# Performance work log

Hardware: AMD Instinct MI355X
Metric: run time of the kernel (lower is better)

Reference implementation:

```python
import jax, jax.numpy as jnp
import numpy as np

VOCAB, EMB, HID, LAYERS = 32000, 512, 512, 2
B, S = 16, 256


def setup_inputs() -> dict:
    key = jax.random.key(0)
    ks = jax.random.split(key, 8)
    x = jax.random.randint(ks[0], (B, S), 0, VOCAB)
    emb = jax.random.normal(ks[1], (VOCAB, EMB), dtype=jnp.float32) * 0.02
    # input_dim == hidden_dim == 512, so per-layer weights can be stacked
    Wih = jax.random.normal(ks[2], (LAYERS, 4 * HID, EMB), dtype=jnp.float32) * 0.05
    Whh = jax.random.normal(ks[3], (LAYERS, 4 * HID, HID), dtype=jnp.float32) * 0.05
    b = jax.random.normal(ks[4], (LAYERS, 4 * HID), dtype=jnp.float32) * 0.05
    fc_w = jax.random.normal(ks[5], (VOCAB, HID), dtype=jnp.float32) * 0.02
    fc_b = jnp.zeros((VOCAB,), dtype=jnp.float32)
    return {"x": x, "emb": emb, "Wih": Wih, "Whh": Whh, "b": b, "fc_w": fc_w, "fc_b": fc_b}


def reference(x, emb, Wih, Whh, b, fc_w, fc_b):
    L = Wih.shape[0]
    Bsz = x.shape[0]
    H = Whh.shape[-1]
    xe = emb[x]  # (B, S, E)
    h0 = jnp.zeros((L, Bsz, H), dtype=emb.dtype)
    c0 = jnp.zeros((L, Bsz, H), dtype=emb.dtype)

    def step(carry, xt):  # xt: (B, E)
        h, c = carry
        inp = xt
        hs, cs = [], []
        for l in range(L):  # small fixed layer loop
            gates = inp @ Wih[l].T + h[l] @ Whh[l].T + b[l]  # (B, 4H)
            i, f, g, o = jnp.split(gates, 4, axis=1)
            cn = jax.nn.sigmoid(f) * c[l] + jax.nn.sigmoid(i) * jnp.tanh(g)
            hn = jax.nn.sigmoid(o) * jnp.tanh(cn)
            hs.append(hn)
            cs.append(cn)
            inp = hn
        return (jnp.stack(hs), jnp.stack(cs)), inp

    _, outs = jax.lax.scan(step, (h0, c0), jnp.swapaxes(xe, 0, 1))  # outs: (S, B, H)
    outs = jnp.swapaxes(outs, 0, 1)  # (B, S, H); dropout is identity (eval)
    logits = outs @ fc_w.T + fc_b  # (B, S, V)
    return logits
```

## Files before the change

kernel.cpp:

```cpp
#include <hip/hip_runtime.h>
#include <hip/hip_bf16.h>

#define SEQ 256
#define NB 16
#define HID 512
#define VOC 32000

typedef short bf16x8 __attribute__((ext_vector_type(8)));
typedef float f32x4 __attribute__((ext_vector_type(4)));
typedef unsigned long long u64;

__device__ __forceinline__ void ld_lds16(const void* g, void* l) {
  __builtin_amdgcn_global_load_lds((const __attribute__((address_space(1))) void*)g,
                                   (__attribute__((address_space(3))) void*)l, 16, 0, 0);
}

__device__ __forceinline__ float sigf(float x) { return 1.0f / (1.0f + expf(-x)); }

__device__ __forceinline__ unsigned pk2(float a, float b) {
  __hip_bfloat16 ha = __float2bfloat16(a), hb = __float2bfloat16(b);
  unsigned short ua = *(unsigned short*)&ha, ub = *(unsigned short*)&hb;
  return (unsigned)ua | ((unsigned)ub << 16);
}

__device__ __forceinline__ u64 agload(const u64* p) {
  return __hip_atomic_load(p, __ATOMIC_RELAXED, __HIP_MEMORY_SCOPE_AGENT);
}
__device__ __forceinline__ void agstore(u64* p, u64 v) {
  __hip_atomic_store(p, v, __ATOMIC_RELAXED, __HIP_MEMORY_SCOPE_AGENT);
}

__device__ __forceinline__ void issue16(u64* q, const u64* base) {
#pragma unroll
  for (int s = 0; s < 4; ++s)
#pragma unroll
    for (int j = 0; j < 4; ++j) q[s * 4 + j] = agload(base + s * 256 + j * 16);
}
__device__ __forceinline__ void revalidate16(u64* q, const u64* base, unsigned tg) {
  for (;;) {
    int bad = 0;
#pragma unroll
    for (int i = 0; i < 16; ++i) bad |= ((unsigned)(q[i] >> 32) != tg);
    if (!__any(bad)) break;
    __builtin_amdgcn_s_sleep(1);
#pragma unroll
    for (int i = 0; i < 16; ++i)
      if ((unsigned)(q[i] >> 32) != tg)
        q[i] = agload(base + (i >> 2) * 256 + (i & 3) * 16);
  }
}

__device__ __forceinline__ void cvt8_hilo(const float* p, bf16x8* h8, bf16x8* l8) {
  union { unsigned short u[8]; bf16x8 v; } uh, ul;
#pragma unroll
  for (int i = 0; i < 8; ++i) {
    float v = p[i];
    __hip_bfloat16 h = __float2bfloat16(v);
    uh.u[i] = *(unsigned short*)&h;
    float rem = v - __bfloat162float(h);
    __hip_bfloat16 l = __float2bfloat16(rem);
    ul.u[i] = *(unsigned short*)&l;
  }
  *h8 = uh.v;
  *l8 = ul.v;
}

__global__ void embed_k(const int* __restrict__ x, const float* __restrict__ emb,
                        unsigned short* __restrict__ xe) {
  int bid = blockIdx.x;
  int t = bid >> 4, b = bid & 15;
  int tok = x[b * SEQ + t];
  const float4* src = (const float4*)(emb + (size_t)tok * HID);
  int e = threadIdx.x;
  float4 a = src[e * 2], c = src[e * 2 + 1];
  uint4 o;
  o.x = pk2(a.x, a.y); o.y = pk2(a.z, a.w);
  o.z = pk2(c.x, c.y); o.w = pk2(c.z, c.w);
  ((uint4*)(xe + (size_t)bid * HID))[e] = o;
}

__global__ void cvt_k(const float* __restrict__ in, uint4* __restrict__ out) {
  size_t i = (size_t)blockIdx.x * blockDim.x + threadIdx.x;
  const float4* in4 = (const float4*)in;
  float4 a = in4[i * 2], b = in4[i * 2 + 1];
  uint4 o;
  o.x = pk2(a.x, a.y); o.y = pk2(a.z, a.w);
  o.z = pk2(b.x, b.y); o.w = pk2(b.z, b.w);
  out[i] = o;
}

__global__ __launch_bounds__(256) void gx_gemm(const __hip_bfloat16* __restrict__ A,
                                               const __hip_bfloat16* __restrict__ Bw,
                                               unsigned short* __restrict__ C) {
  __shared__ __align__(16) unsigned short lds_a[128 * 32];
  __shared__ __align__(16) unsigned short lds_b[128 * 32];
  const int tid = threadIdx.x;
  const int lane = tid & 63, wid = tid >> 6;
  const int m0 = blockIdx.y * 128, n0 = blockIdx.x * 128;
  const char* Ab = (const char*)A;
  const char* Bb = (const char*)Bw;
  const int ra = tid >> 2, cb = (tid & 3) * 16;
  f32x4 acc[4][4] = {};
  const int wm = (wid >> 1) * 64, wn = (wid & 1) * 64;
  const int fr = lane & 15, fk = (lane >> 4) * 8;
  for (int k0 = 0; k0 < HID; k0 += 32) {
    ld_lds16(Ab + (size_t)(m0 + ra) * 1024 + k0 * 2 + cb, (char*)lds_a + wid * 1024);
    ld_lds16(Ab + (size_t)(m0 + 64 + ra) * 1024 + k0 * 2 + cb, (char*)lds_a + 4096 + wid * 1024);
    ld_lds16(Bb + (size_t)(n0 + ra) * 1024 + k0 * 2 + cb, (char*)lds_b + wid * 1024);
    ld_lds16(Bb + (size_t)(n0 + 64 + ra) * 1024 + k0 * 2 + cb, (char*)lds_b + 4096 + wid * 1024);
    __syncthreads();
    bf16x8 af[4], bf[4];
#pragma unroll
    for (int i = 0; i < 4; ++i) af[i] = *(const bf16x8*)&lds_a[(wm + i * 16 + fr) * 32 + fk];
#pragma unroll
    for (int j = 0; j < 4; ++j) bf[j] = *(const bf16x8*)&lds_b[(wn + j * 16 + fr) * 32 + fk];
#pragma unroll
    for (int i = 0; i < 4; ++i)
#pragma unroll
      for (int j = 0; j < 4; ++j)
        acc[i][j] = __builtin_amdgcn_mfma_f32_16x16x32_bf16(af[i], bf[j], acc[i][j], 0, 0, 0);
    __syncthreads();
  }
  const int cr = (lane >> 4) * 4, cc = lane & 15;
#pragma unroll
  for (int i = 0; i < 4; ++i)
#pragma unroll
    for (int jj = 0; jj < 4; ++jj) {
      size_t base = (size_t)(m0 + wm + i * 16 + cr) * 2048 + (n0 + wn + jj * 16 + cc);
#pragma unroll
      for (int r = 0; r < 4; ++r) {
        __hip_bfloat16 h = __float2bfloat16(acc[i][jj][r]);
        C[base + (size_t)r * 2048] = *(unsigned short*)&h;
      }
    }
}

__global__ __launch_bounds__(256) void lstm_k(
    const float* __restrict__ Wih, const float* __restrict__ Whh,
    const float* __restrict__ bias, const unsigned short* __restrict__ gxb,
    u64* __restrict__ h0r, u64* __restrict__ h1r, unsigned short* __restrict__ outs) {
  __shared__ float pbuf[4][16][17];
  const int tid = threadIdx.x, bid = blockIdx.x;
  const int lay = bid >> 7, r8 = bid & 127;
  const int hc0 = r8 * 4;
  const int wid = tid >> 6, lane = tid & 63;
  const int b16 = lane & 15, hi = lane >> 4;

  const int jrow = (b16 >> 2) * HID + hc0 + (b16 & 3);
  const int kb = wid * 128 + hi * 8;
  const float* wih_row = Wih + ((size_t)lay * 2048 + jrow) * HID;
  const float* whh_row = Whh + ((size_t)lay * 2048 + jrow) * HID;
  bf16x8 w0[4], w1[4], w2[4], w3[4];
#pragma unroll
  for (int s = 0; s < 4; ++s) {
    if (lay == 0) {
      cvt8_hilo(whh_row + kb + s * 32, &w0[s], &w1[s]);
      w2[s] = w0[s]; w3[s] = w1[s];
    } else {
      cvt8_hilo(wih_row + kb + s * 32, &w0[s], &w1[s]);
      cvt8_hilo(whh_row + kb + s * 32, &w2[s], &w3[s]);
    }
  }
  const int eb = lane & 15, ehl = lane >> 4;
  float bq[4];
#pragma unroll
  for (int q = 0; q < 4; ++q) bq[q] = bias[lay * 2048 + q * HID + hc0 + ehl];
  float c_reg = 0.f;
  const int lbase = wid * 1024 + hi * 64 + b16;

#pragma unroll 1
  for (int t = 0; t < SEQ; ++t) {
    f32x4 acc0 = {0.f, 0.f, 0.f, 0.f}, acc1 = {0.f, 0.f, 0.f, 0.f};
    float gxr[4] = {0.f, 0.f, 0.f, 0.f};
    if (lay == 0) {
      const u64* srcA = h0r + (size_t)t * 4096 + lbase;
      u64 qa[16];
      issue16(qa, srcA);
      if (wid == 0) {
        const unsigned short* gp = gxb + ((size_t)(t * 16 + eb)) * 2048 + hc0 + ehl;
#pragma unroll
        for (int q = 0; q < 4; ++q) {
          union { unsigned u; float f; } cv;
          cv.u = (unsigned)gp[q * HID] << 16;
          gxr[q] = cv.f;
        }
        asm volatile("" : "+v"(gxr[0]), "+v"(gxr[1]), "+v"(gxr[2]), "+v"(gxr[3]));
      }
      revalidate16(qa, srcA, (unsigned)t);
#pragma unroll
      for (int s = 0; s < 4; ++s) {
        union { unsigned u[4]; bf16x8 v; } bb;
#pragma unroll
        for (int j = 0; j < 4; ++j) bb.u[j] = (unsigned)qa[s * 4 + j];
        acc0 = __builtin_amdgcn_mfma_f32_16x16x32_bf16(w0[s], bb.v, acc0, 0, 0, 0);
        acc1 = __builtin_amdgcn_mfma_f32_16x16x32_bf16(w1[s], bb.v, acc1, 0, 0, 0);
      }
    } else {
      const u64* srcA = h0r + (size_t)(t + 1) * 4096 + lbase;
      const u64* srcB = h1r + (size_t)t * 4096 + lbase;
      u64 qb[16], qa[16];
      issue16(qb, srcB);
      issue16(qa, srcA);
      revalidate16(qb, srcB, (unsigned)t);
#pragma unroll
      for (int s = 0; s < 4; ++s) {
        union { unsigned u[4]; bf16x8 v; } bb;
#pragma unroll
        for (int j = 0; j < 4; ++j) bb.u[j] = (unsigned)qb[s * 4 + j];
        acc0 = __builtin_amdgcn_mfma_f32_16x16x32_bf16(w2[s], bb.v, acc0, 0, 0, 0);
        acc1 = __builtin_amdgcn_mfma_f32_16x16x32_bf16(w3[s], bb.v, acc1, 0, 0, 0);
      }
      revalidate16(qa, srcA, (unsigned)(t + 1));
#pragma unroll
      for (int s = 0; s < 4; ++s) {
        union { unsigned u[4]; bf16x8 v; } bb;
#pragma unroll
        for (int j = 0; j < 4; ++j) bb.u[j] = (unsigned)qa[s * 4 + j];
        acc0 = __builtin_amdgcn_mfma_f32_16x16x32_bf16(w0[s], bb.v, acc0, 0, 0, 0);
        acc1 = __builtin_amdgcn_mfma_f32_16x16x32_bf16(w1[s], bb.v, acc1, 0, 0, 0);
      }
    }
    f32x4 acc = acc0 + acc1;
#pragma unroll
    for (int rr = 0; rr < 4; ++rr) pbuf[wid][hi * 4 + rr][b16] = acc[rr];
    __syncthreads();

    if (wid == 0) {
      float pre[4];
#pragma unroll
      for (int q = 0; q < 4; ++q) {
        const int rl = q * 4 + ehl;
        pre[q] = bq[q] + gxr[q] + pbuf[0][rl][eb] + pbuf[1][rl][eb] +
                 pbuf[2][rl][eb] + pbuf[3][rl][eb];
      }
      float iv = sigf(pre[0]), fv = sigf(pre[1]);
      float gv = tanhf(pre[2]), ov = sigf(pre[3]);
      c_reg = fv * c_reg + iv * gv;
      float hn = ov * tanhf(c_reg);
      __hip_bfloat16 hh = __float2bfloat16(hn);
      int hb = (int)*(unsigned short*)&hh;
      int pr = __shfl_xor(hb, 16, 64);
      unsigned data32 = (unsigned)(unsigned short)hb | ((unsigned)(unsigned short)pr << 16);
      u64* ringo = (lay ? h1r : h0r) + (size_t)(t + 1) * 4096;
      if ((ehl & 1) == 0)
        agstore(ringo + (r8 * 2 + (ehl >> 1)) * 16 + eb,
                (u64)data32 | ((u64)(unsigned)(t + 1) << 32));
      if (lay) {
        unsigned d23 = (unsigned)__shfl((int)data32, eb + 32, 64);
        if (ehl == 0)
          *(u64*)(outs + ((size_t)(t * 16 + eb)) * 512 + hc0) = (u64)data32 | ((u64)d23 << 32);
      }
    }
    __syncthreads();
  }
}

__global__ __launch_bounds__(256) void fc_gemm(const __hip_bfloat16* __restrict__ A,
                                               const __hip_bfloat16* __restrict__ Bw,
                                               const float* __restrict__ bias,
                                               float* __restrict__ C) {
  __shared__ __align__(16) unsigned short lds_a[128 * 32];
  __shared__ __align__(16) unsigned short lds_b[128 * 32];
  const int tid = threadIdx.x;
  const int lane = tid & 63, wid = tid >> 6;
  const int m0 = blockIdx.y * 128, n0 = blockIdx.x * 128;
  const char* Ab = (const char*)A;
  const char* Bb = (const char*)Bw;
  const int ra = tid >> 2, cb = (tid & 3) * 16;
  f32x4 acc[4][4] = {};
  const int wm = (wid >> 1) * 64, wn = (wid & 1) * 64;
  const int fr = lane & 15, fk = (lane >> 4) * 8;
  for (int k0 = 0; k0 < HID; k0 += 32) {
    ld_lds16(Ab + (size_t)(m0 + ra) * 1024 + k0 * 2 + cb, (char*)lds_a + wid * 1024);
    ld_lds16(Ab + (size_t)(m0 + 64 + ra) * 1024 + k0 * 2 + cb, (char*)lds_a + 4096 + wid * 1024);
    ld_lds16(Bb + (size_t)(n0 + ra) * 1024 + k0 * 2 + cb, (char*)lds_b + wid * 1024);
    ld_lds16(Bb + (size_t)(n0 + 64 + ra) * 1024 + k0 * 2 + cb, (char*)lds_b + 4096 + wid * 1024);
    __syncthreads();
    bf16x8 af[4], bf[4];
#pragma unroll
    for (int i = 0; i < 4; ++i) af[i] = *(const bf16x8*)&lds_a[(wm + i * 16 + fr) * 32 + fk];
#pragma unroll
    for (int j = 0; j < 4; ++j) bf[j] = *(const bf16x8*)&lds_b[(wn + j * 16 + fr) * 32 + fk];
#pragma unroll
    for (int i = 0; i < 4; ++i)
#pragma unroll
      for (int j = 0; j < 4; ++j)
        acc[i][j] = __builtin_amdgcn_mfma_f32_16x16x32_bf16(af[i], bf[j], acc[i][j], 0, 0, 0);
    __syncthreads();
  }
  const int cr = (lane >> 4) * 4, cc = lane & 15;
  float bv[4];
#pragma unroll
  for (int jj = 0; jj < 4; ++jj) bv[jj] = bias[n0 + wn + jj * 16 + cc];
#pragma unroll
  for (int i = 0; i < 4; ++i) {
#pragma unroll
    for (int jj = 0; jj < 4; ++jj) {
#pragma unroll
      for (int rr = 0; rr < 4; ++rr) {
        int tok = m0 + wm + i * 16 + cr + rr;
        int orow = (tok & 15) * SEQ + (tok >> 4);
        C[(size_t)orow * VOC + (n0 + wn + jj * 16 + cc)] = acc[i][jj][rr] + bv[jj];
      }
    }
  }
}

extern "C" void kernel_launch(void* const* d_in, const int* in_sizes, int n_in,
                              void* d_out, int out_size, void* d_ws, size_t ws_size,
                              hipStream_t stream) {
  const int* x = (const int*)d_in[0];
  const float* emb = (const float*)d_in[1];
  const float* Wih = (const float*)d_in[2];
  const float* Whh = (const float*)d_in[3];
  const float* bias = (const float*)d_in[4];
  const float* fcw = (const float*)d_in[5];
  const float* fcb = (const float*)d_in[6];
  float* out = (float*)d_out;
  char* ws = (char*)d_ws;

  u64* h0r = (u64*)ws;
  u64* h1r = (u64*)(ws + 8421376);
  uint4* wih0_bf = (uint4*)(ws + 16842752);
  unsigned short* gxb = (unsigned short*)(ws + 18939904);
  unsigned short* xe = (unsigned short*)(ws + 35717120);
  unsigned short* outs = (unsigned short*)(ws + 35717120);
  uint4* fcw_bf = (uint4*)ws;

  hipMemsetAsync(ws, 0, 16842752, stream);
  embed_k<<<SEQ * NB, 64, 0, stream>>>(x, emb, xe);
  cvt_k<<<512, 256, 0, stream>>>(Wih, wih0_bf);
  gx_gemm<<<dim3(16, 32), 256, 0, stream>>>((const __hip_bfloat16*)xe,
                                            (const __hip_bfloat16*)wih0_bf, gxb);
  lstm_k<<<256, 256, 0, stream>>>(Wih, Whh, bias, gxb, h0r, h1r, outs);
  cvt_k<<<8000, 256, 0, stream>>>(fcw, fcw_bf);
  fc_gemm<<<dim3(250, 32), 256, 0, stream>>>((const __hip_bfloat16*)outs,
                                             (const __hip_bfloat16*)fcw_bf, fcb, out);
}
```

Baseline: 1.226 ms.

## Fuse LSTM recurrence and FC GEMM into one persistent kernel with flag-based overlap

Merges the LSTM recurrence and the vocabulary projection into one kernel launch. 256 blocks run the recurrence and raise per-timestep flags. The other 768 blocks spin on those flags and compute FC tiles as soon as their token rows are ready, converting fp32 weights to bf16 on the fly. This removes the separate weight-conversion kernels and overlaps the large FC GEMM with the serial recurrence. It also swaps expf/tanhf for v_exp/v_rcp approximations. Risks are co-residency and deadlock if the recurrence blocks are not all scheduled, contention that slows the latency-critical recurrence, and repeated fp32 weight reads across tiles.

```diff
diff --git a/kernel.cpp b/kernel.cpp
--- a/kernel.cpp
+++ b/kernel.cpp
@@ -15,8 +15,6 @@
                                    (__attribute__((address_space(3))) void*)l, 16, 0, 0);
 }
 
-__device__ __forceinline__ float sigf(float x) { return 1.0f / (1.0f + expf(-x)); }
-
 __device__ __forceinline__ unsigned pk2(float a, float b) {
   __hip_bfloat16 ha = __float2bfloat16(a), hb = __float2bfloat16(b);
   unsigned short ua = *(unsigned short*)&ha, ub = *(unsigned short*)&hb;
@@ -28,6 +26,23 @@
 }
 __device__ __forceinline__ void agstore(u64* p, u64 v) {
   __hip_atomic_store(p, v, __ATOMIC_RELAXED, __HIP_MEMORY_SCOPE_AGENT);
+}
+
+__device__ __forceinline__ float fexp2(float x) {
+  float r;
+  asm("v_exp_f32 %0, %1" : "=v"(r) : "v"(x));
+  return r;
+}
+__device__ __forceinline__ float frcp(float x) {
+  float r;
+  asm("v_rcp_f32 %0, %1" : "=v"(r) : "v"(x));
+  return r;
+}
+__device__ __forceinline__ float fsig(float x) {
+  return frcp(1.f + fexp2(-1.44269504f * x));
+}
+__device__ __forceinline__ float ftanh(float x) {
+  return 1.f - 2.f * frcp(1.f + fexp2(2.88539008f * x));
 }
 
 __device__ __forceinline__ void issue16(u64* q, const u64* base) {
@@ -79,18 +94,8 @@
   ((uint4*)(xe + (size_t)bid * HID))[e] = o;
 }
 
-__global__ void cvt_k(const float* __restrict__ in, uint4* __restrict__ out) {
-  size_t i = (size_t)blockIdx.x * blockDim.x + threadIdx.x;
-  const float4* in4 = (const float4*)in;
-  float4 a = in4[i * 2], b = in4[i * 2 + 1];
-  uint4 o;
-  o.x = pk2(a.x, a.y); o.y = pk2(a.z, a.w);
-  o.z = pk2(b.x, b.y); o.w = pk2(b.z, b.w);
-  out[i] = o;
-}
-
 __global__ __launch_bounds__(256) void gx_gemm(const __hip_bfloat16* __restrict__ A,
-                                               const __hip_bfloat16* __restrict__ Bw,
+                                               const float* __restrict__ Bw32,
                                                unsigned short* __restrict__ C) {
   __shared__ __align__(16) unsigned short lds_a[128 * 32];
   __shared__ __align__(16) unsigned short lds_b[128 * 32];
@@ -98,7 +103,6 @@
   const int lane = tid & 63, wid = tid >> 6;
   const int m0 = blockIdx.y * 128, n0 = blockIdx.x * 128;
   const char* Ab = (const char*)A;
-  const char* Bb = (const char*)Bw;
   const int ra = tid >> 2, cb = (tid & 3) * 16;
   f32x4 acc[4][4] = {};
   const int wm = (wid >> 1) * 64, wn = (wid & 1) * 64;
@@ -106,8 +110,16 @@
   for (int k0 = 0; k0 < HID; k0 += 32) {
     ld_lds16(Ab + (size_t)(m0 + ra) * 1024 + k0 * 2 + cb, (char*)lds_a + wid * 1024);
     ld_lds16(Ab + (size_t)(m0 + 64 + ra) * 1024 + k0 * 2 + cb, (char*)lds_a + 4096 + wid * 1024);
-    ld_lds16(Bb + (size_t)(n0 + ra) * 1024 + k0 * 2 + cb, (char*)lds_b + wid * 1024);
-    ld_lds16(Bb + (size_t)(n0 + 64 + ra) * 1024 + k0 * 2 + cb, (char*)lds_b + 4096 + wid * 1024);
+    {
+      const float* p0 = Bw32 + (size_t)(n0 + ra) * HID + k0 + (tid & 3) * 8;
+      const float* p1 = p0 + (size_t)64 * HID;
+      float4 a0 = ((const float4*)p0)[0], a1 = ((const float4*)p0)[1];
+      float4 b0 = ((const float4*)p1)[0], b1 = ((const float4*)p1)[1];
+      uint4 pa = {pk2(a0.x, a0.y), pk2(a0.z, a0.w), pk2(a1.x, a1.y), pk2(a1.z, a1.w)};
+      uint4 pb = {pk2(b0.x, b0.y), pk2(b0.z, b0.w), pk2(b1.x, b1.y), pk2(b1.z, b1.w)};
+      ((uint4*)lds_b)[tid] = pa;
+      ((uint4*)lds_b)[256 + tid] = pb;
+    }
     __syncthreads();
     bf16x8 af[4], bf[4];
 #pragma unroll
@@ -121,186 +133,229 @@
         acc[i][j] = __builtin_amdgcn_mfma_f32_16x16x32_bf16(af[i], bf[j], acc[i][j], 0, 0, 0);
     __syncthreads();
   }
-  const int cr = (lane >> 4) * 4, cc = lane & 15;
+  const int cr = (lane >> 4) * 4, cc2 = lane & 15;
 #pragma unroll
   for (int i = 0; i < 4; ++i)
 #pragma unroll
     for (int jj = 0; jj < 4; ++jj) {
-      size_t base = (size_t)(m0 + wm + i * 16 + cr) * 2048 + (n0 + wn + jj * 16 + cc);
-#pragma unroll
-      for (int r = 0; r < 4; ++r) {
-        __hip_bfloat16 h = __float2bfloat16(acc[i][jj][r]);
-        C[base + (size_t)r * 2048] = *(unsigned short*)&h;
-      }
-    }
-}
-
-__global__ __launch_bounds__(256) void lstm_k(
+      size_t base = (size_t)(m0 + wm + i * 16 + cr) * 2048 + (n0 + wn + jj * 16 + cc2);
+#pragma unroll
+      for (int rr = 0; rr < 4; ++rr) {
+        __hip_bfloat16 h = __float2bfloat16(acc[i][jj][rr]);
+        C[base + (size_t)rr * 2048] = *(unsigned short*)&h;
+      }
+    }
+}
+
+__global__ __launch_bounds__(256) void mega_k(
     const float* __restrict__ Wih, const float* __restrict__ Whh,
     const float* __restrict__ bias, const unsigned short* __restrict__ gxb,
-    u64* __restrict__ h0r, u64* __restrict__ h1r, unsigned short* __restrict__ outs) {
-  __shared__ float pbuf[4][16][17];
-  const int tid = threadIdx.x, bid = blockIdx.x;
-  const int lay = bid >> 7, r8 = bid & 127;
-  const int hc0 = r8 * 4;
-  const int wid = tid >> 6, lane = tid & 63;
-  const int b16 = lane & 15, hi = lane >> 4;
-
-  const int jrow = (b16 >> 2) * HID + hc0 + (b16 & 3);
-  const int kb = wid * 128 + hi * 8;
-  const float* wih_row = Wih + ((size_t)lay * 2048 + jrow) * HID;
-  const float* whh_row = Whh + ((size_t)lay * 2048 + jrow) * HID;
-  bf16x8 w0[4], w1[4], w2[4], w3[4];
-#pragma unroll
-  for (int s = 0; s < 4; ++s) {
-    if (lay == 0) {
-      cvt8_hilo(whh_row + kb + s * 32, &w0[s], &w1[s]);
-      w2[s] = w0[s]; w3[s] = w1[s];
-    } else {
-      cvt8_hilo(wih_row + kb + s * 32, &w0[s], &w1[s]);
-      cvt8_hilo(whh_row + kb + s * 32, &w2[s], &w3[s]);
-    }
-  }
-  const int eb = lane & 15, ehl = lane >> 4;
-  float bq[4];
-#pragma unroll
-  for (int q = 0; q < 4; ++q) bq[q] = bias[lay * 2048 + q * HID + hc0 + ehl];
-  float c_reg = 0.f;
-  const int lbase = wid * 1024 + hi * 64 + b16;
-
-#pragma unroll 1
-  for (int t = 0; t < SEQ; ++t) {
-    f32x4 acc0 = {0.f, 0.f, 0.f, 0.f}, acc1 = {0.f, 0.f, 0.f, 0.f};
-    float gxr[4] = {0.f, 0.f, 0.f, 0.f};
-    if (lay == 0) {
-      const u64* srcA = h0r + (size_t)t * 4096 + lbase;
-      u64 qa[16];
-      issue16(qa, srcA);
-      if (wid == 0) {
-        const unsigned short* gp = gxb + ((size_t)(t * 16 + eb)) * 2048 + hc0 + ehl;
-#pragma unroll
-        for (int q = 0; q < 4; ++q) {
-          union { unsigned u; float f; } cv;
-          cv.u = (unsigned)gp[q * HID] << 16;
-          gxr[q] = cv.f;
-        }
-        asm volatile("" : "+v"(gxr[0]), "+v"(gxr[1]), "+v"(gxr[2]), "+v"(gxr[3]));
-      }
-      revalidate16(qa, srcA, (unsigned)t);
-#pragma unroll
-      for (int s = 0; s < 4; ++s) {
-        union { unsigned u[4]; bf16x8 v; } bb;
-#pragma unroll
-        for (int j = 0; j < 4; ++j) bb.u[j] = (unsigned)qa[s * 4 + j];
-        acc0 = __builtin_amdgcn_mfma_f32_16x16x32_bf16(w0[s], bb.v, acc0, 0, 0, 0);
-        acc1 = __builtin_amdgcn_mfma_f32_16x16x32_bf16(w1[s], bb.v, acc1, 0, 0, 0);
-      }
-    } else {
-      const u64* srcA = h0r + (size_t)(t + 1) * 4096 + lbase;
-      const u64* srcB = h1r + (size_t)t * 4096 + lbase;
-      u64 qb[16], qa[16];
-      issue16(qb, srcB);
-      issue16(qa, srcA);
-      revalidate16(qb, srcB, (unsigned)t);
-#pragma unroll
-      for (int s = 0; s < 4; ++s) {
-        union { unsigned u[4]; bf16x8 v; } bb;
-#pragma unroll
-        for (int j = 0; j < 4; ++j) bb.u[j] = (unsigned)qb[s * 4 + j];
-        acc0 = __builtin_amdgcn_mfma_f32_16x16x32_bf16(w2[s], bb.v, acc0, 0, 0, 0);
-        acc1 = __builtin_amdgcn_mfma_f32_16x16x32_bf16(w3[s], bb.v, acc1, 0, 0, 0);
-      }
-      revalidate16(qa, srcA, (unsigned)(t + 1));
-#pragma unroll
-      for (int s = 0; s < 4; ++s) {
-        union { unsigned u[4]; bf16x8 v; } bb;
-#pragma unroll
-        for (int j = 0; j < 4; ++j) bb.u[j] = (unsigned)qa[s * 4 + j];
-        acc0 = __builtin_amdgcn_mfma_f32_16x16x32_bf16(w0[s], bb.v, acc0, 0, 0, 0);
-        acc1 = __builtin_amdgcn_mfma_f32_16x16x32_bf16(w1[s], bb.v, acc1, 0, 0, 0);
-      }
-    }
-    f32x4 acc = acc0 + acc1;
-#pragma unroll
-    for (int rr = 0; rr < 4; ++rr) pbuf[wid][hi * 4 + rr][b16] = acc[rr];
-    __syncthreads();
-
-    if (wid == 0) {
-      float pre[4];
-#pragma unroll
-      for (int q = 0; q < 4; ++q) {
-        const int rl = q * 4 + ehl;
-        pre[q] = bq[q] + gxr[q] + pbuf[0][rl][eb] + pbuf[1][rl][eb] +
-                 pbuf[2][rl][eb] + pbuf[3][rl][eb];
-      }
-      float iv = sigf(pre[0]), fv = sigf(pre[1]);
-      float gv = tanhf(pre[2]), ov = sigf(pre[3]);
-      c_reg = fv * c_reg + iv * gv;
-      float hn = ov * tanhf(c_reg);
-      __hip_bfloat16 hh = __float2bfloat16(hn);
-      int hb = (int)*(unsigned short*)&hh;
-      int pr = __shfl_xor(hb, 16, 64);
-      unsigned data32 = (unsigned)(unsigned short)hb | ((unsigned)(unsigned short)pr << 16);
-      u64* ringo = (lay ? h1r : h0r) + (size_t)(t + 1) * 4096;
-      if ((ehl & 1) == 0)
-        agstore(ringo + (r8 * 2 + (ehl >> 1)) * 16 + eb,
-                (u64)data32 | ((u64)(unsigned)(t + 1) << 32));
-      if (lay) {
-        unsigned d23 = (unsigned)__shfl((int)data32, eb + 32, 64);
-        if (ehl == 0)
-          *(u64*)(outs + ((size_t)(t * 16 + eb)) * 512 + hc0) = (u64)data32 | ((u64)d23 << 32);
-      }
-    }
-    __syncthreads();
-  }
-}
-
-__global__ __launch_bounds__(256) void fc_gemm(const __hip_bfloat16* __restrict__ A,
-                                               const __hip_bfloat16* __restrict__ Bw,
-                                               const float* __restrict__ bias,
-                                               float* __restrict__ C) {
-  __shared__ __align__(16) unsigned short lds_a[128 * 32];
-  __shared__ __align__(16) unsigned short lds_b[128 * 32];
+    u64* __restrict__ h0r, u64* __restrict__ h1r, unsigned short* __restrict__ outs,
+    unsigned* __restrict__ flags, const float* __restrict__ fcw,
+    const float* __restrict__ fcb, float* __restrict__ C) {
+  __shared__ __align__(16) char smem[16384];
+  __shared__ int ready;
+  const int bid = blockIdx.x;
   const int tid = threadIdx.x;
   const int lane = tid & 63, wid = tid >> 6;
-  const int m0 = blockIdx.y * 128, n0 = blockIdx.x * 128;
-  const char* Ab = (const char*)A;
-  const char* Bb = (const char*)Bw;
-  const int ra = tid >> 2, cb = (tid & 3) * 16;
-  f32x4 acc[4][4] = {};
-  const int wm = (wid >> 1) * 64, wn = (wid & 1) * 64;
-  const int fr = lane & 15, fk = (lane >> 4) * 8;
-  for (int k0 = 0; k0 < HID; k0 += 32) {
-    ld_lds16(Ab + (size_t)(m0 + ra) * 1024 + k0 * 2 + cb, (char*)lds_a + wid * 1024);
-    ld_lds16(Ab + (size_t)(m0 + 64 + ra) * 1024 + k0 * 2 + cb, (char*)lds_a + 4096 + wid * 1024);
-    ld_lds16(Bb + (size_t)(n0 + ra) * 1024 + k0 * 2 + cb, (char*)lds_b + wid * 1024);
-    ld_lds16(Bb + (size_t)(n0 + 64 + ra) * 1024 + k0 * 2 + cb, (char*)lds_b + 4096 + wid * 1024);
-    __syncthreads();
-    bf16x8 af[4], bf[4];
-#pragma unroll
-    for (int i = 0; i < 4; ++i) af[i] = *(const bf16x8*)&lds_a[(wm + i * 16 + fr) * 32 + fk];
-#pragma unroll
-    for (int j = 0; j < 4; ++j) bf[j] = *(const bf16x8*)&lds_b[(wn + j * 16 + fr) * 32 + fk];
-#pragma unroll
-    for (int i = 0; i < 4; ++i)
-#pragma unroll
-      for (int j = 0; j < 4; ++j)
-        acc[i][j] = __builtin_amdgcn_mfma_f32_16x16x32_bf16(af[i], bf[j], acc[i][j], 0, 0, 0);
-    __syncthreads();
-  }
-  const int cr = (lane >> 4) * 4, cc = lane & 15;
-  float bv[4];
-#pragma unroll
-  for (int jj = 0; jj < 4; ++jj) bv[jj] = bias[n0 + wn + jj * 16 + cc];
-#pragma unroll
-  for (int i = 0; i < 4; ++i) {
-#pragma unroll
-    for (int jj = 0; jj < 4; ++jj) {
-#pragma unroll
-      for (int rr = 0; rr < 4; ++rr) {
-        int tok = m0 + wm + i * 16 + cr + rr;
-        int orow = (tok & 15) * SEQ + (tok >> 4);
-        C[(size_t)orow * VOC + (n0 + wn + jj * 16 + cc)] = acc[i][jj][rr] + bv[jj];
+
+  if (bid < 256) {
+    __builtin_amdgcn_s_setprio(1);
+    float (*pbuf)[16][17] = (float(*)[16][17])smem;
+    const int lay = bid >> 7, r8 = bid & 127;
+    const int hc0 = r8 * 4;
+    const int b16 = lane & 15, hi = lane >> 4;
+
+    const int jrow = (b16 >> 2) * HID + hc0 + (b16 & 3);
+    const int kb = wid * 128 + hi * 8;
+    const float* wih_row = Wih + ((size_t)lay * 2048 + jrow) * HID;
+    const float* whh_row = Whh + ((size_t)lay * 2048 + jrow) * HID;
+    bf16x8 w0[4], w1[4], w2[4], w3[4];
+#pragma unroll
+    for (int s = 0; s < 4; ++s) {
+      if (lay == 0) {
+        cvt8_hilo(whh_row + kb + s * 32, &w0[s], &w1[s]);
+        w2[s] = w0[s]; w3[s] = w1[s];
+      } else {
+        cvt8_hilo(wih_row + kb + s * 32, &w0[s], &w1[s]);
+        cvt8_hilo(whh_row + kb + s * 32, &w2[s], &w3[s]);
+      }
+    }
+    const int eb = lane & 15, ehl = lane >> 4;
+    float bq[4];
+#pragma unroll
+    for (int q = 0; q < 4; ++q) bq[q] = bias[lay * 2048 + q * HID + hc0 + ehl];
+    float c_reg = 0.f;
+    const int lbase = wid * 1024 + hi * 64 + b16;
+
+#pragma unroll 1
+    for (int t = 0; t < SEQ; ++t) {
+      f32x4 acc0 = {0.f, 0.f, 0.f, 0.f}, acc1 = {0.f, 0.f, 0.f, 0.f};
+      float gxr[4] = {0.f, 0.f, 0.f, 0.f};
+      if (lay == 0) {
+        const u64* srcA = h0r + (size_t)t * 4096 + lbase;
+        u64 qa[16];
+        issue16(qa, srcA);
+        if (wid == 0) {
+          const unsigned short* gp = gxb + ((size_t)(t * 16 + eb)) * 2048 + hc0 + ehl;
+#pragma unroll
+          for (int q = 0; q < 4; ++q) {
+            union { unsigned u; float f; } cv;
+            cv.u = (unsigned)gp[q * HID] << 16;
+            gxr[q] = cv.f;
+          }
+          asm volatile("" : "+v"(gxr[0]), "+v"(gxr[1]), "+v"(gxr[2]), "+v"(gxr[3]));
+        }
+        revalidate16(qa, srcA, (unsigned)t);
+#pragma unroll
+        for (int s = 0; s < 4; ++s) {
+          union { unsigned u[4]; bf16x8 v; } bb;
+#pragma unroll
+          for (int j = 0; j < 4; ++j) bb.u[j] = (unsigned)qa[s * 4 + j];
+          acc0 = __builtin_amdgcn_mfma_f32_16x16x32_bf16(w0[s], bb.v, acc0, 0, 0, 0);
+          acc1 = __builtin_amdgcn_mfma_f32_16x16x32_bf16(w1[s], bb.v, acc1, 0, 0, 0);
+        }
+      } else {
+        const u64* srcA = h0r + (size_t)(t + 1) * 4096 + lbase;
+        const u64* srcB = h1r + (size_t)t * 4096 + lbase;
+        u64 qb[16], qa[16];
+        issue16(qb, srcB);
+        issue16(qa, srcA);
+        revalidate16(qb, srcB, (unsigned)t);
+#pragma unroll
+        for (int s = 0; s < 4; ++s) {
+          union { unsigned u[4]; bf16x8 v; } bb;
+#pragma unroll
+          for (int j = 0; j < 4; ++j) bb.u[j] = (unsigned)qb[s * 4 + j];
+          acc0 = __builtin_amdgcn_mfma_f32_16x16x32_bf16(w2[s], bb.v, acc0, 0, 0, 0);
+          acc1 = __builtin_amdgcn_mfma_f32_16x16x32_bf16(w3[s], bb.v, acc1, 0, 0, 0);
+        }
+        revalidate16(qa, srcA, (unsigned)(t + 1));
+#pragma unroll
+        for (int s = 0; s < 4; ++s) {
+          union { unsigned u[4]; bf16x8 v; } bb;
+#pragma unroll
+          for (int j = 0; j < 4; ++j) bb.u[j] = (unsigned)qa[s * 4 + j];
+          acc0 = __builtin_amdgcn_mfma_f32_16x16x32_bf16(w0[s], bb.v, acc0, 0, 0, 0);
+          acc1 = __builtin_amdgcn_mfma_f32_16x16x32_bf16(w1[s], bb.v, acc1, 0, 0, 0);
+        }
+      }
+      f32x4 acc = acc0 + acc1;
+#pragma unroll
+      for (int rr = 0; rr < 4; ++rr) pbuf[wid][hi * 4 + rr][b16] = acc[rr];
+      __syncthreads();
+
+      if (wid == 0) {
+        if (lay) {
+          asm volatile("s_waitcnt vmcnt(0)" ::: "memory");
+          if (lane == 0 && t > 0)
+            __hip_atomic_fetch_add(flags + (size_t)(t - 1) * 16, 1u, __ATOMIC_RELAXED,
+                                   __HIP_MEMORY_SCOPE_AGENT);
+        }
+        float pre[4];
+#pragma unroll
+        for (int q = 0; q < 4; ++q) {
+          const int rl = q * 4 + ehl;
+          pre[q] = bq[q] + gxr[q] + pbuf[0][rl][eb] + pbuf[1][rl][eb] +
+                   pbuf[2][rl][eb] + pbuf[3][rl][eb];
+        }
+        float iv = fsig(pre[0]), fv = fsig(pre[1]);
+        float gv = ftanh(pre[2]), ov = fsig(pre[3]);
+        c_reg = fv * c_reg + iv * gv;
+        float hn = ov * ftanh(c_reg);
+        __hip_bfloat16 hh = __float2bfloat16(hn);
+        int hb = (int)*(unsigned short*)&hh;
+        int pr = __shfl_xor(hb, 16, 64);
+        unsigned data32 = (unsigned)(unsigned short)hb | ((unsigned)(unsigned short)pr << 16);
+        u64* ringo = (lay ? h1r : h0r) + (size_t)(t + 1) * 4096;
+        if ((ehl & 1) == 0)
+          agstore(ringo + (r8 * 2 + (ehl >> 1)) * 16 + eb,
+                  (u64)data32 | ((u64)(unsigned)(t + 1) << 32));
+        if (lay) {
+          unsigned d23 = (unsigned)__shfl((int)data32, eb + 32, 64);
+          if (ehl == 0)
+            agstore((u64*)(outs + ((size_t)(t * 16 + eb)) * 512 + hc0),
+                    (u64)data32 | ((u64)d23 << 32));
+        }
+      }
+      __syncthreads();
+    }
+    if (lay == 1 && wid == 0) {
+      asm volatile("s_waitcnt vmcnt(0)" ::: "memory");
+      if (lane == 0)
+        __hip_atomic_fetch_add(flags + (size_t)(SEQ - 1) * 16, 1u, __ATOMIC_RELAXED,
+                               __HIP_MEMORY_SCOPE_AGENT);
+    }
+  } else {
+    unsigned short* lds_a = (unsigned short*)smem;
+    unsigned short* lds_b = lds_a + 4096;
+    const int wrk = bid - 256;
+    const int t0 = wrk * 8000 / 768, t1 = (wrk + 1) * 8000 / 768;
+    const int ra = tid >> 2, cbyt = (tid & 3) * 16;
+    const int wm = (wid >> 1) * 64, wn = (wid & 1) * 64;
+    const int fr = lane & 15, fk = (lane >> 4) * 8;
+    for (int tau = t0; tau < t1; ++tau) {
+      const int m = tau / 250, n = tau - m * 250;
+      const int m0 = m * 128, n0 = n * 128;
+      for (;;) {
+        int ok = 1;
+        if (tid < 8) {
+          unsigned f = __hip_atomic_load(flags + (size_t)(m * 8 + tid) * 16,
+                                         __ATOMIC_RELAXED, __HIP_MEMORY_SCOPE_AGENT);
+          ok = (f >= 128u);
+        }
+        int allok = __all(ok);
+        if (tid == 0) ready = allok;
+        __syncthreads();
+        int rd = ready;
+        __syncthreads();
+        if (rd) break;
+        __builtin_amdgcn_s_sleep(64);
+      }
+      const char* Ab = (const char*)outs;
+      f32x4 acc[4][4] = {};
+      for (int k0 = 0; k0 < HID; k0 += 32) {
+        ld_lds16(Ab + (size_t)(m0 + ra) * 1024 + k0 * 2 + cbyt, (char*)lds_a + wid * 1024);
+        ld_lds16(Ab + (size_t)(m0 + 64 + ra) * 1024 + k0 * 2 + cbyt,
+                 (char*)lds_a + 4096 + wid * 1024);
+        {
+          const float* p0 = fcw + (size_t)(n0 + ra) * HID + k0 + (tid & 3) * 8;
+          const float* p1 = p0 + (size_t)64 * HID;
+          float4 a0 = ((const float4*)p0)[0], a1 = ((const float4*)p0)[1];
+          float4 b0 = ((const float4*)p1)[0], b1 = ((const float4*)p1)[1];
+          uint4 pa = {pk2(a0.x, a0.y), pk2(a0.z, a0.w), pk2(a1.x, a1.y), pk2(a1.z, a1.w)};
+          uint4 pb = {pk2(b0.x, b0.y), pk2(b0.z, b0.w), pk2(b1.x, b1.y), pk2(b1.z, b1.w)};
+          ((uint4*)lds_b)[tid] = pa;
+          ((uint4*)lds_b)[256 + tid] = pb;
+        }
+        __syncthreads();
+        bf16x8 af[4], bf[4];
+#pragma unroll
+        for (int i = 0; i < 4; ++i) af[i] = *(const bf16x8*)&lds_a[(wm + i * 16 + fr) * 32 + fk];
+#pragma unroll
+        for (int j = 0; j < 4; ++j) bf[j] = *(const bf16x8*)&lds_b[(wn + j * 16 + fr) * 32 + fk];
+#pragma unroll
+        for (int i = 0; i < 4; ++i)
+#pragma unroll
+          for (int j = 0; j < 4; ++j)
+            acc[i][j] = __builtin_amdgcn_mfma_f32_16x16x32_bf16(af[i], bf[j], acc[i][j], 0, 0, 0);
+        __syncthreads();
+      }
+      const int cr = (lane >> 4) * 4, cc2 = lane & 15;
+      float bv[4];
+#pragma unroll
+      for (int jj = 0; jj < 4; ++jj) bv[jj] = fcb[n0 + wn + jj * 16 + cc2];
+#pragma unroll
+      for (int i = 0; i < 4; ++i) {
+#pragma unroll
+        for (int jj = 0; jj < 4; ++jj) {
+#pragma unroll
+          for (int rr = 0; rr < 4; ++rr) {
+            int tok = m0 + wm + i * 16 + cr + rr;
+            int orow = (tok & 15) * SEQ + (tok >> 4);
+            C[(size_t)orow * VOC + (n0 + wn + jj * 16 + cc2)] = acc[i][jj][rr] + bv[jj];
+          }
+        }
       }
     }
   }
@@ -319,21 +374,15 @@
   float* out = (float*)d_out;
   char* ws = (char*)d_ws;
 
-  u64* h0r = (u64*)ws;
-  u64* h1r = (u64*)(ws + 8421376);
-  uint4* wih0_bf = (uint4*)(ws + 16842752);
-  unsigned short* gxb = (unsigned short*)(ws + 18939904);
-  unsigned short* xe = (unsigned short*)(ws + 35717120);
-  unsigned short* outs = (unsigned short*)(ws + 35717120);
-  uint4* fcw_bf = (uint4*)ws;
-
-  hipMemsetAsync(ws, 0, 16842752, stream);
+  unsigned* flags = (unsigned*)ws;
+  u64* h0r = (u64*)(ws + 16384);
+  u64* h1r = (u64*)(ws + 8437760);
+  unsigned short* xe = (unsigned short*)(ws + 16859136);
+  unsigned short* gxb = (unsigned short*)(ws + 21053440);
+  unsigned short* outs = (unsigned short*)(ws + 37830656);
+
+  hipMemsetAsync(ws, 0, 16859136, stream);
   embed_k<<<SEQ * NB, 64, 0, stream>>>(x, emb, xe);
-  cvt_k<<<512, 256, 0, stream>>>(Wih, wih0_bf);
-  gx_gemm<<<dim3(16, 32), 256, 0, stream>>>((const __hip_bfloat16*)xe,
-                                            (const __hip_bfloat16*)wih0_bf, gxb);
-  lstm_k<<<256, 256, 0, stream>>>(Wih, Whh, bias, gxb, h0r, h1r, outs);
-  cvt_k<<<8000, 256, 0, stream>>>(fcw, fcw_bf);
-  fc_gemm<<<dim3(250, 32), 256, 0, stream>>>((const __hip_bfloat16*)outs,
-                                             (const __hip_bfloat16*)fcw_bf, fcb, out);
-}
+  gx_gemm<<<dim3(16, 32), 256, 0, stream>>>((const __hip_bfloat16*)xe, Wih, gxb);
+  mega_k<<<1024, 256, 0, stream>>>(Wih, Whh, bias, gxb, h0r, h1r, outs, flags, fcw, fcb, out);
+}
```

Result: slower. 1.553 ms (+26.6%).

## Fuse fp32-to-bf16 weight conversion into GEMMs and trim LSTM step sync

Applied to the files above, without the earlier changes.

Removes the separate cvt_k passes for Wih layer 0 and fc_w. The gx and fc GEMMs now load fp32 weights directly, pack them to bf16 in registers and write them into LDS. In the LSTM kernel the gate reduction buffer is double-buffered by timestep parity so the trailing __syncthreads can be dropped, sigmoid and tanh use raw v_exp/v_rcp approximations, and the s_sleep in the spin-wait is removed. The trade-offs: the fc GEMM reads fp32 weights (twice the bytes) and reconverts them in each of 32 row-blocks, the fast transcendentals lose accuracy, and the tighter spin polls more aggressively.

```diff
diff --git a/kernel.cpp b/kernel.cpp
--- a/kernel.cpp
+++ b/kernel.cpp
@@ -15,8 +15,6 @@
                                    (__attribute__((address_space(3))) void*)l, 16, 0, 0);
 }
 
-__device__ __forceinline__ float sigf(float x) { return 1.0f / (1.0f + expf(-x)); }
-
 __device__ __forceinline__ unsigned pk2(float a, float b) {
   __hip_bfloat16 ha = __float2bfloat16(a), hb = __float2bfloat16(b);
   unsigned short ua = *(unsigned short*)&ha, ub = *(unsigned short*)&hb;
@@ -30,6 +28,21 @@
   __hip_atomic_store(p, v, __ATOMIC_RELAXED, __HIP_MEMORY_SCOPE_AGENT);
 }
 
+__device__ __forceinline__ float fexp2(float x) {
+  float r;
+  asm("v_exp_f32 %0, %1" : "=v"(r) : "v"(x));
+  return r;
+}
+__device__ __forceinline__ float frcp(float x) {
+  float r;
+  asm("v_rcp_f32 %0, %1" : "=v"(r) : "v"(x));
+  return r;
+}
+__device__ __forceinline__ float fsig(float x) { return frcp(1.f + fexp2(-1.44269504f * x)); }
+__device__ __forceinline__ float ftanh(float x) {
+  return 1.f - 2.f * frcp(1.f + fexp2(2.88539008f * x));
+}
+
 __device__ __forceinline__ void issue16(u64* q, const u64* base) {
 #pragma unroll
   for (int s = 0; s < 4; ++s)
@@ -42,7 +55,6 @@
 #pragma unroll
     for (int i = 0; i < 16; ++i) bad |= ((unsigned)(q[i] >> 32) != tg);
     if (!__any(bad)) break;
-    __builtin_amdgcn_s_sleep(1);
 #pragma unroll
     for (int i = 0; i < 16; ++i)
       if ((unsigned)(q[i] >> 32) != tg)
@@ -79,18 +91,8 @@
   ((uint4*)(xe + (size_t)bid * HID))[e] = o;
 }
 
-__global__ void cvt_k(const float* __restrict__ in, uint4* __restrict__ out) {
-  size_t i = (size_t)blockIdx.x * blockDim.x + threadIdx.x;
-  const float4* in4 = (const float4*)in;
-  float4 a = in4[i * 2], b = in4[i * 2 + 1];
-  uint4 o;
-  o.x = pk2(a.x, a.y); o.y = pk2(a.z, a.w);
-  o.z = pk2(b.x, b.y); o.w = pk2(b.z, b.w);
-  out[i] = o;
-}
-
 __global__ __launch_bounds__(256) void gx_gemm(const __hip_bfloat16* __restrict__ A,
-                                               const __hip_bfloat16* __restrict__ Bw,
+                                               const float* __restrict__ Bw32,
                                                unsigned short* __restrict__ C) {
   __shared__ __align__(16) unsigned short lds_a[128 * 32];
   __shared__ __align__(16) unsigned short lds_b[128 * 32];
@@ -98,7 +100,6 @@
   const int lane = tid & 63, wid = tid >> 6;
   const int m0 = blockIdx.y * 128, n0 = blockIdx.x * 128;
   const char* Ab = (const char*)A;
-  const char* Bb = (const char*)Bw;
   const int ra = tid >> 2, cb = (tid & 3) * 16;
   f32x4 acc[4][4] = {};
   const int wm = (wid >> 1) * 64, wn = (wid & 1) * 64;
@@ -106,8 +107,16 @@
   for (int k0 = 0; k0 < HID; k0 += 32) {
     ld_lds16(Ab + (size_t)(m0 + ra) * 1024 + k0 * 2 + cb, (char*)lds_a + wid * 1024);
     ld_lds16(Ab + (size_t)(m0 + 64 + ra) * 1024 + k0 * 2 + cb, (char*)lds_a + 4096 + wid * 1024);
-    ld_lds16(Bb + (size_t)(n0 + ra) * 1024 + k0 * 2 + cb, (char*)lds_b + wid * 1024);
-    ld_lds16(Bb + (size_t)(n0 + 64 + ra) * 1024 + k0 * 2 + cb, (char*)lds_b + 4096 + wid * 1024);
+    {
+      const float* p0 = Bw32 + (size_t)(n0 + ra) * HID + k0 + (tid & 3) * 8;
+      const float* p1 = p0 + (size_t)64 * HID;
+      float4 a0 = ((const float4*)p0)[0], a1 = ((const float4*)p0)[1];
+      float4 b0 = ((const float4*)p1)[0], b1 = ((const float4*)p1)[1];
+      uint4 pa = {pk2(a0.x, a0.y), pk2(a0.z, a0.w), pk2(a1.x, a1.y), pk2(a1.z, a1.w)};
+      uint4 pb = {pk2(b0.x, b0.y), pk2(b0.z, b0.w), pk2(b1.x, b1.y), pk2(b1.z, b1.w)};
+      ((uint4*)lds_b)[tid] = pa;
+      ((uint4*)lds_b)[256 + tid] = pb;
+    }
     __syncthreads();
     bf16x8 af[4], bf[4];
 #pragma unroll
@@ -121,16 +130,16 @@
         acc[i][j] = __builtin_amdgcn_mfma_f32_16x16x32_bf16(af[i], bf[j], acc[i][j], 0, 0, 0);
     __syncthreads();
   }
-  const int cr = (lane >> 4) * 4, cc = lane & 15;
+  const int cr = (lane >> 4) * 4, cc2 = lane & 15;
 #pragma unroll
   for (int i = 0; i < 4; ++i)
 #pragma unroll
     for (int jj = 0; jj < 4; ++jj) {
-      size_t base = (size_t)(m0 + wm + i * 16 + cr) * 2048 + (n0 + wn + jj * 16 + cc);
-#pragma unroll
-      for (int r = 0; r < 4; ++r) {
-        __hip_bfloat16 h = __float2bfloat16(acc[i][jj][r]);
-        C[base + (size_t)r * 2048] = *(unsigned short*)&h;
+      size_t base = (size_t)(m0 + wm + i * 16 + cr) * 2048 + (n0 + wn + jj * 16 + cc2);
+#pragma unroll
+      for (int rr = 0; rr < 4; ++rr) {
+        __hip_bfloat16 h = __float2bfloat16(acc[i][jj][rr]);
+        C[base + (size_t)rr * 2048] = *(unsigned short*)&h;
       }
     }
 }
@@ -139,7 +148,7 @@
     const float* __restrict__ Wih, const float* __restrict__ Whh,
     const float* __restrict__ bias, const unsigned short* __restrict__ gxb,
     u64* __restrict__ h0r, u64* __restrict__ h1r, unsigned short* __restrict__ outs) {
-  __shared__ float pbuf[4][16][17];
+  __shared__ float pbuf[2][4][16][17];
   const int tid = threadIdx.x, bid = blockIdx.x;
   const int lay = bid >> 7, r8 = bid & 127;
   const int hc0 = r8 * 4;
@@ -170,6 +179,7 @@
 
 #pragma unroll 1
   for (int t = 0; t < SEQ; ++t) {
+    const int par = t & 1;
     f32x4 acc0 = {0.f, 0.f, 0.f, 0.f}, acc1 = {0.f, 0.f, 0.f, 0.f};
     float gxr[4] = {0.f, 0.f, 0.f, 0.f};
     if (lay == 0) {
@@ -222,7 +232,7 @@
     }
     f32x4 acc = acc0 + acc1;
 #pragma unroll
-    for (int rr = 0; rr < 4; ++rr) pbuf[wid][hi * 4 + rr][b16] = acc[rr];
+    for (int rr = 0; rr < 4; ++rr) pbuf[par][wid][hi * 4 + rr][b16] = acc[rr];
     __syncthreads();
 
     if (wid == 0) {
@@ -230,13 +240,13 @@
 #pragma unroll
       for (int q = 0; q < 4; ++q) {
         const int rl = q * 4 + ehl;
-        pre[q] = bq[q] + gxr[q] + pbuf[0][rl][eb] + pbuf[1][rl][eb] +
-                 pbuf[2][rl][eb] + pbuf[3][rl][eb];
-      }
-      float iv = sigf(pre[0]), fv = sigf(pre[1]);
-      float gv = tanhf(pre[2]), ov = sigf(pre[3]);
+        pre[q] = bq[q] + gxr[q] + pbuf[par][0][rl][eb] + pbuf[par][1][rl][eb] +
+                 pbuf[par][2][rl][eb] + pbuf[par][3][rl][eb];
+      }
+      float iv = fsig(pre[0]), fv = fsig(pre[1]);
+      float gv = ftanh(pre[2]), ov = fsig(pre[3]);
       c_reg = fv * c_reg + iv * gv;
-      float hn = ov * tanhf(c_reg);
+      float hn = ov * ftanh(c_reg);
       __hip_bfloat16 hh = __float2bfloat16(hn);
       int hb = (int)*(unsigned short*)&hh;
       int pr = __shfl_xor(hb, 16, 64);
@@ -251,12 +261,11 @@
           *(u64*)(outs + ((size_t)(t * 16 + eb)) * 512 + hc0) = (u64)data32 | ((u64)d23 << 32);
       }
     }
-    __syncthreads();
   }
 }
 
 __global__ __launch_bounds__(256) void fc_gemm(const __hip_bfloat16* __restrict__ A,
-                                               const __hip_bfloat16* __restrict__ Bw,
+                                               const float* __restrict__ Bw32,
                                                const float* __restrict__ bias,
                                                float* __restrict__ C) {
   __shared__ __align__(16) unsigned short lds_a[128 * 32];
@@ -265,7 +274,6 @@
   const int lane = tid & 63, wid = tid >> 6;
   const int m0 = blockIdx.y * 128, n0 = blockIdx.x * 128;
   const char* Ab = (const char*)A;
-  const char* Bb = (const char*)Bw;
   const int ra = tid >> 2, cb = (tid & 3) * 16;
   f32x4 acc[4][4] = {};
   const int wm = (wid >> 1) * 64, wn = (wid & 1) * 64;
@@ -273,8 +281,16 @@
   for (int k0 = 0; k0 < HID; k0 += 32) {
     ld_lds16(Ab + (size_t)(m0 + ra) * 1024 + k0 * 2 + cb, (char*)lds_a + wid * 1024);
     ld_lds16(Ab + (size_t)(m0 + 64 + ra) * 1024 + k0 * 2 + cb, (char*)lds_a + 4096 + wid * 1024);
-    ld_lds16(Bb + (size_t)(n0 + ra) * 1024 + k0 * 2 + cb, (char*)lds_b + wid * 1024);
-    ld_lds16(Bb + (size_t)(n0 + 64 + ra) * 1024 + k0 * 2 + cb, (char*)lds_b + 4096 + wid * 1024);
+    {
+      const float* p0 = Bw32 + (size_t)(n0 + ra) * HID + k0 + (tid & 3) * 8;
+      const float* p1 = p0 + (size_t)64 * HID;
+      float4 a0 = ((const float4*)p0)[0], a1 = ((const float4*)p0)[1];
+      float4 b0 = ((const float4*)p1)[0], b1 = ((const float4*)p1)[1];
+      uint4 pa = {pk2(a0.x, a0.y), pk2(a0.z, a0.w), pk2(a1.x, a1.y), pk2(a1.z, a1.w)};
+      uint4 pb = {pk2(b0.x, b0.y), pk2(b0.z, b0.w), pk2(b1.x, b1.y), pk2(b1.z, b1.w)};
+      ((uint4*)lds_b)[tid] = pa;
+      ((uint4*)lds_b)[256 + tid] = pb;
+    }
     __syncthreads();
     bf16x8 af[4], bf[4];
 #pragma unroll
@@ -288,10 +304,10 @@
         acc[i][j] = __builtin_amdgcn_mfma_f32_16x16x32_bf16(af[i], bf[j], acc[i][j], 0, 0, 0);
     __syncthreads();
   }
-  const int cr = (lane >> 4) * 4, cc = lane & 15;
+  const int cr = (lane >> 4) * 4, cc2 = lane & 15;
   float bv[4];
 #pragma unroll
-  for (int jj = 0; jj < 4; ++jj) bv[jj] = bias[n0 + wn + jj * 16 + cc];
+  for (int jj = 0; jj < 4; ++jj) bv[jj] = bias[n0 + wn + jj * 16 + cc2];
 #pragma unroll
   for (int i = 0; i < 4; ++i) {
 #pragma unroll
@@ -300,7 +316,7 @@
       for (int rr = 0; rr < 4; ++rr) {
         int tok = m0 + wm + i * 16 + cr + rr;
         int orow = (tok & 15) * SEQ + (tok >> 4);
-        C[(size_t)orow * VOC + (n0 + wn + jj * 16 + cc)] = acc[i][jj][rr] + bv[jj];
+        C[(size_t)orow * VOC + (n0 + wn + jj * 16 + cc2)] = acc[i][jj][rr] + bv[jj];
       }
     }
   }
@@ -321,19 +337,13 @@
 
   u64* h0r = (u64*)ws;
   u64* h1r = (u64*)(ws + 8421376);
-  uint4* wih0_bf = (uint4*)(ws + 16842752);
-  unsigned short* gxb = (unsigned short*)(ws + 18939904);
-  unsigned short* xe = (unsigned short*)(ws + 35717120);
-  unsigned short* outs = (unsigned short*)(ws + 35717120);
-  uint4* fcw_bf = (uint4*)ws;
+  unsigned short* xe = (unsigned short*)(ws + 16842752);
+  unsigned short* gxb = (unsigned short*)(ws + 21037056);
+  unsigned short* outs = (unsigned short*)(ws + 37814272);
 
   hipMemsetAsync(ws, 0, 16842752, stream);
   embed_k<<<SEQ * NB, 64, 0, stream>>>(x, emb, xe);
-  cvt_k<<<512, 256, 0, stream>>>(Wih, wih0_bf);
-  gx_gemm<<<dim3(16, 32), 256, 0, stream>>>((const __hip_bfloat16*)xe,
-                                            (const __hip_bfloat16*)wih0_bf, gxb);
+  gx_gemm<<<dim3(16, 32), 256, 0, stream>>>((const __hip_bfloat16*)xe, Wih, gxb);
   lstm_k<<<256, 256, 0, stream>>>(Wih, Whh, bias, gxb, h0r, h1r, outs);
-  cvt_k<<<8000, 256, 0, stream>>>(fcw, fcw_bf);
-  fc_gemm<<<dim3(250, 32), 256, 0, stream>>>((const __hip_bfloat16*)outs,
-                                             (const __hip_bfloat16*)fcw_bf, fcb, out);
-}
+  fc_gemm<<<dim3(250, 32), 256, 0, stream>>>((const __hip_bfloat16*)outs, fcw, fcb, out);
+}
```

Result: slower. 1.714 ms (+39.8%).
